# Optimization experiments

Hardware: AMD Instinct MI355X
Metric: run time of the kernel (lower is better)

The kernel has to match this reference:

```python
import jax, jax.numpy as jnp
import numpy as np

B, S, F, DV, H, DH, L = 32, 600, 9, 1024, 16, 64, 2


def setup_inputs() -> dict:
    key = jax.random.key(0)
    ks = jax.random.split(key, 24)
    w = lambda k, shape, s=0.05: jax.random.normal(k, shape, dtype=jnp.float32) * s
    return {
        "x": w(ks[0], (B, S, F), 1.0),
        "enc_in_W": w(ks[1], (F, DV)), "enc_in_b": w(ks[2], (DV,)),
        "Wq": w(ks[3], (L, H, DV, DH)), "bq": w(ks[4], (L, H, DH)),
        "Wk": w(ks[5], (L, H, DV, DH)), "bk": w(ks[6], (L, H, DH)),
        "Wv": w(ks[7], (L, H, DV, DH)), "bv": w(ks[8], (L, H, DH)),
        "Wo": w(ks[9], (L, DV, DV)), "bo": w(ks[10], (L, DV)),
        "W1": w(ks[11], (L, DV, DV)), "b1": w(ks[12], (L, DV)),
        "W2": w(ks[13], (L, DV, DV)), "b2": w(ks[14], (L, DV)),
        "ln1_w": jnp.ones((L, DV)), "ln1_b": jnp.zeros((L, DV)),
        "ln2_w": jnp.ones((L, DV)), "ln2_b": jnp.zeros((L, DV)),
        "out_W": w(ks[15], (DV, F)), "out_b": w(ks[16], (F,)),
    }


def _layernorm(v, g, b):
    mu = v.mean(-1, keepdims=True)
    var = v.var(-1, keepdims=True)  # biased, matches torch LayerNorm
    return (v - mu) / jnp.sqrt(var + 1e-5) * g + b


def reference(x, enc_in_W, enc_in_b, Wq, bq, Wk, bk, Wv, bv, Wo, bo,
              W1, b1, W2, b2, ln1_w, ln1_b, ln2_w, ln2_b, out_W, out_b):
    # enc_input_fc; pe skipped (code checks pe_mode == 'stardard', never true)
    h = x @ enc_in_W + enc_in_b  # [B,S,DV]
    scale = 1.0 / jnp.sqrt(jnp.float32(DH))
    for l in range(L):
        q = jnp.einsum('bsd,hdk->bhsk', h, Wq[l]) + bq[l][None, :, None, :]
        k = jnp.einsum('bsd,hdk->bhsk', h, Wk[l]) + bk[l][None, :, None, :]
        v = jnp.einsum('bsd,hdk->bhsk', h, Wv[l]) + bv[l][None, :, None, :]
        attn = jax.nn.softmax(jnp.einsum('bhsk,bhtk->bhst', q, k) * scale, axis=-1)
        ctx = jnp.einsum('bhst,bhtk->bhsk', attn, v)  # [B,H,S,DH]
        # torch: stack(heads, dim=-1) -> [B,S,DH,H], then flatten(start_dim=2)
        a = ctx.transpose(0, 2, 3, 1).reshape(B, S, DH * H)
        attn_out = a @ Wo[l] + bo[l]
        x1 = _layernorm(h + attn_out, ln1_w[l], ln1_b[l])
        ff = jax.nn.elu(x1 @ W2[l] + b2[l]) @ W1[l] + b1[l]  # fc1(elu(fc2(x1)))
        h = _layernorm(x1 + ff, ln2_w[l], ln2_b[l])
    out = h @ out_W + out_b  # [B,S,F]; in_seq_len == out_seq_len -> no out_seq_fc
    return out
```

## Files before the change

kernel.cpp:

```cpp
#include <hip/hip_runtime.h>

typedef unsigned short u16;
typedef unsigned int u32;
typedef __attribute__((ext_vector_type(8))) short shortx8;
typedef __attribute__((ext_vector_type(4))) float floatx4;
typedef __attribute__((ext_vector_type(4))) u32 uintx4;
typedef __attribute__((ext_vector_type(2))) u32 uintx2;

#define AS1 __attribute__((address_space(1)))
#define AS3 __attribute__((address_space(3)))

__device__ __forceinline__ float bf2f(u16 u) {
  return __builtin_bit_cast(float, ((u32)u) << 16);
}
__device__ __forceinline__ u16 f2bf(float f) {
  u32 i = __builtin_bit_cast(u32, f);
  u32 r = (i + 0x7fffu + ((i >> 16) & 1u)) >> 16;
  return (u16)r;
}
__device__ __forceinline__ u16 f2bf_rtz(float f) {
  return (u16)(__builtin_bit_cast(u32, f) >> 16);
}

__launch_bounds__(256)
__global__ void pack_all(const float* __restrict__ Wq, const float* __restrict__ Wk,
                         const float* __restrict__ Wv, const float* __restrict__ Wo,
                         const float* __restrict__ W1, const float* __restrict__ W2,
                         const float* __restrict__ bq, const float* __restrict__ bk,
                         const float* __restrict__ bv,
                         u16* __restrict__ Bqkv, u16* __restrict__ Bwo,
                         u16* __restrict__ Bw1, u16* __restrict__ Bw2,
                         float* __restrict__ bias) {
  __shared__ u16 T[64 * 72];
  const int blk = blockIdx.x;
  const int t = threadIdx.x;

  if (blk < 1536) {
    const int which = blk >> 9, r = blk & 511;
    const int kt = r & 15, y = r >> 4;
    const float* W = (which == 0) ? Wq : (which == 1) ? Wk : Wv;
    u16* dst = Bqkv + (size_t)which * 1048576;
    const int l = y >> 4, h = y & 15;
    const int rr = t >> 2, cq = (t & 3) * 16;
    const float* src = W + ((size_t)y * 1024 + kt * 64 + rr) * 64 + cq;
#pragma unroll
    for (int e4 = 0; e4 < 4; ++e4) {
      float4 f = *(const float4*)(src + e4 * 4);
      T[(cq + e4 * 4 + 0) * 72 + rr] = f2bf(f.x);
      T[(cq + e4 * 4 + 1) * 72 + rr] = f2bf(f.y);
      T[(cq + e4 * 4 + 2) * 72 + rr] = f2bf(f.z);
      T[(cq + e4 * 4 + 3) * 72 + rr] = f2bf(f.w);
    }
    __syncthreads();
    const int dd = t >> 2, kq = (t & 3) * 16;
    u16* drow = dst + (size_t)l * 3145728 + ((size_t)h * 64 + dd) * 1024 + kt * 64 + kq;
    *(uintx4*)(drow) = *(const uintx4*)&T[dd * 72 + kq];
    *(uintx4*)(drow + 8) = *(const uintx4*)&T[dd * 72 + kq + 8];
  } else if (blk < 2048) {
    const int r = blk - 1536;
    const int l = r >> 8, rx = r & 255;
    const int rt = rx >> 4, nt = rx & 15;
    const int rr = t >> 2, cq = (t & 3) * 16;
    const float* src = Wo + (size_t)l * 1048576 + (size_t)(rt * 64 + rr) * 1024 + nt * 64 + cq;
#pragma unroll
    for (int e4 = 0; e4 < 4; ++e4) {
      float4 f = *(const float4*)(src + e4 * 4);
      T[(cq + e4 * 4 + 0) * 72 + rr] = f2bf(f.x);
      T[(cq + e4 * 4 + 1) * 72 + rr] = f2bf(f.y);
      T[(cq + e4 * 4 + 2) * 72 + rr] = f2bf(f.z);
      T[(cq + e4 * 4 + 3) * 72 + rr] = f2bf(f.w);
    }
    __syncthreads();
    const int hh = t & 15;
#pragma unroll
    for (int pass = 0; pass < 4; ++pass) {
      const int nl = pass * 16 + (t >> 4);
      uintx2 pk;
      u16 v0 = T[nl * 72 + 0 * 16 + hh], v1 = T[nl * 72 + 1 * 16 + hh];
      u16 v2 = T[nl * 72 + 2 * 16 + hh], v3 = T[nl * 72 + 3 * 16 + hh];
      pk[0] = (u32)v0 | ((u32)v1 << 16);
      pk[1] = (u32)v2 | ((u32)v3 << 16);
      *(uintx2*)&Bwo[(size_t)l * 1048576 + (size_t)(nt * 64 + nl) * 1024 + hh * 64 + rt * 4] = pk;
    }
  } else if (blk < 3072) {
    const int job = (blk - 2048) >> 9;
    const int r = (blk - 2048) & 511;
    const float* W = job == 0 ? W1 : W2;
    u16* dst = job == 0 ? Bw1 : Bw2;
    const int l = r >> 8, rx = r & 255;
    const int ct = rx & 15, rt = rx >> 4;
    const int rr = t >> 2, cq = (t & 3) * 16;
    const float* src = W + (size_t)l * 1048576 + (size_t)(rt * 64 + rr) * 1024 + ct * 64 + cq;
#pragma unroll
    for (int e4 = 0; e4 < 4; ++e4) {
      float4 f = *(const float4*)(src + e4 * 4);
      T[(cq + e4 * 4 + 0) * 72 + rr] = f2bf(f.x);
      T[(cq + e4 * 4 + 1) * 72 + rr] = f2bf(f.y);
      T[(cq + e4 * 4 + 2) * 72 + rr] = f2bf(f.z);
      T[(cq + e4 * 4 + 3) * 72 + rr] = f2bf(f.w);
    }
    __syncthreads();
    const int cc = t >> 2, rq = (t & 3) * 16;
    u16* drow = dst + (size_t)l * 1048576 + (size_t)(ct * 64 + cc) * 1024 + rt * 64 + rq;
    *(uintx4*)(drow) = *(const uintx4*)&T[cc * 72 + rq];
    *(uintx4*)(drow + 8) = *(const uintx4*)&T[cc * 72 + rq + 8];
  } else {
    const int i = (blk - 3072) * 256 + t;
    const int l = i / 3072, n = i % 3072;
    const int which = n >> 10, nn = n & 1023;
    const float* s = (which == 0) ? bq : (which == 1) ? bk : bv;
    bias[i] = s[l * 1024 + nn];
  }
}

__launch_bounds__(256)
__global__ void enc_kernel(const float* __restrict__ x, const float* __restrict__ W,
                           const float* __restrict__ bias, u16* __restrict__ h) {
  const size_t i = (size_t)blockIdx.x * 256 + threadIdx.x;
  const int m = (int)(i >> 7), nq = (int)((i & 127) << 3);
  const float* xr = x + (size_t)m * 9;
  float xv[9];
#pragma unroll
  for (int f = 0; f < 9; ++f) xv[f] = xr[f];
  u16 ov[8];
#pragma unroll
  for (int e = 0; e < 8; ++e) {
    float acc = bias[nq + e];
#pragma unroll
    for (int f = 0; f < 9; ++f) acc += xv[f] * W[f * 1024 + nq + e];
    ov[e] = f2bf(acc);
  }
  *(uintx4*)&h[(size_t)m * 1024 + nq] = *(const uintx4*)ov;
}

template <int EPI>
__launch_bounds__(512)
__global__ void gemm_bt_wide(const u16* __restrict__ A, int lda,
                             const u16* __restrict__ Bt,
                             const float* __restrict__ bias,
                             const u16* __restrict__ R, int ldr,
                             u16* __restrict__ C, int ldc) {
  constexpr int K = 1024;
  __shared__ u16 As[128 * 64];
  __shared__ u16 Bs[256 * 64];
  const int tid = threadIdx.x;
  const int lane = tid & 63;
  const int w = tid >> 6;
  const int wr = w >> 2, wc = w & 3;
  const int m0 = blockIdx.y * 128, n0 = blockIdx.x * 256;

  floatx4 acc[4][4];
#pragma unroll
  for (int i = 0; i < 4; ++i)
#pragma unroll
    for (int j = 0; j < 4; ++j) acc[i][j] = (floatx4){0.f, 0.f, 0.f, 0.f};

  const u16* Ab = A + (size_t)m0 * lda;
  const u16* Bb = Bt + (size_t)n0 * K;

  for (int k0 = 0; k0 < K; k0 += 64) {
#pragma unroll
    for (int p = 0; p < 2; ++p) {
      const int o = p * 8192 + tid * 16;
      const int row = o >> 7;
      const int ke = (o & 127) >> 1;
      __builtin_amdgcn_global_load_lds((const AS1 void*)(Ab + (size_t)row * lda + (k0 + ke)),
                                       (AS3 void*)((char*)As + o), 16, 0, 0);
    }
#pragma unroll
    for (int p = 0; p < 4; ++p) {
      const int o = p * 8192 + tid * 16;
      const int row = o >> 7;
      const int ke = (o & 127) >> 1;
      __builtin_amdgcn_global_load_lds((const AS1 void*)(Bb + (size_t)row * K + (k0 + ke)),
                                       (AS3 void*)((char*)Bs + o), 16, 0, 0);
    }
    __syncthreads();
#pragma unroll
    for (int ks = 0; ks < 2; ++ks) {
      shortx8 af[4], bfr[4];
#pragma unroll
      for (int i = 0; i < 4; ++i) {
        const int ar = wr * 64 + i * 16 + (lane & 15);
        af[i] = *(const shortx8*)&As[ar * 64 + ks * 32 + (lane >> 4) * 8];
        const int br = wc * 64 + i * 16 + (lane & 15);
        bfr[i] = *(const shortx8*)&Bs[br * 64 + ks * 32 + (lane >> 4) * 8];
      }
#pragma unroll
      for (int i = 0; i < 4; ++i)
#pragma unroll
        for (int j = 0; j < 4; ++j)
          acc[i][j] = __builtin_amdgcn_mfma_f32_16x16x32_bf16(af[i], bfr[j], acc[i][j], 0, 0, 0);
    }
    __syncthreads();
  }

  const int lr = (lane >> 4) * 4, lc = lane & 15;
#pragma unroll
  for (int i = 0; i < 4; ++i) {
#pragma unroll
    for (int j = 0; j < 4; ++j) {
      const int col = n0 + wc * 64 + j * 16 + lc;
      const float bv = bias[col];
      const bool qcol = (EPI == 3) && (col < 1024);
#pragma unroll
      for (int r = 0; r < 4; ++r) {
        const int row = m0 + wr * 64 + i * 16 + lr + r;
        float v = acc[i][j][r] + bv;
        if (EPI == 1) v += bf2f(R[(size_t)row * ldr + col]);
        if (EPI == 2) v = v > 0.f ? v : expm1f(v);
        if (EPI == 3 && qcol) v *= 0.125f;
        C[(size_t)row * ldc + col] = f2bf(v);
      }
    }
  }
}

__launch_bounds__(256)
__global__ void attn_mfma(const u16* __restrict__ qkv, u16* __restrict__ aout) {
  const int qt = blockIdx.x, bh = blockIdx.y;
  const int b = bh >> 4, h = bh & 15;
  const int tid = threadIdx.x, lane = tid & 63, w = tid >> 6;
  const int g = lane >> 4, lq = lane & 15;

  __shared__ u16 K_ld[128 * 72];
  __shared__ u16 Vt[64 * 136];
  __shared__ u16 P_ld[4][16 * 136];

  const size_t bbase = (size_t)b * 600 * 3072;
  const int q0 = qt * 128 + w * 32;
  const int tloc = tid >> 1, dhalf = (tid & 1) * 32;
  const int dq = w * 16;

  shortx8 aq[2][2];
#pragma unroll
  for (int sub = 0; sub < 2; ++sub) {
    const int s = q0 + sub * 16 + lq;
    if (s < 600) {
      const u16* qp = qkv + bbase + (size_t)s * 3072 + h * 64 + g * 8;
      aq[sub][0] = *(const shortx8*)qp;
      aq[sub][1] = *(const shortx8*)(qp + 32);
    } else {
      aq[sub][0] = (shortx8){0, 0, 0, 0, 0, 0, 0, 0};
      aq[sub][1] = (shortx8){0, 0, 0, 0, 0, 0, 0, 0};
    }
  }

  floatx4 Oa[2][4];
  float m[2][4], l[2][4];
#pragma unroll
  for (int sub = 0; sub < 2; ++sub) {
#pragma unroll
    for (int db = 0; db < 4; ++db) Oa[sub][db] = (floatx4){0.f, 0.f, 0.f, 0.f};
#pragma unroll
    for (int r = 0; r < 4; ++r) { m[sub][r] = -1e30f; l[sub][r] = 0.f; }
  }

  uintx4 kreg[4];
  shortx8 vra, vrb, vrc, vrd;

  auto LOADC = [&](int ch) {
    const int t0 = ch * 128;
    if (ch < 4) {
      const u16* kp = qkv + bbase + (size_t)(t0 + tloc) * 3072 + 1024 + h * 64 + dhalf;
#pragma unroll
      for (int c = 0; c < 4; ++c) kreg[c] = *(const uintx4*)(kp + c * 8);
      const u16* vp0 = qkv + bbase + (size_t)(t0 + lane * 2) * 3072 + 2048 + h * 64 + dq;
      vra = *(const shortx8*)vp0;
      vrb = *(const shortx8*)(vp0 + 8);
      vrc = *(const shortx8*)(vp0 + 3072);
      vrd = *(const shortx8*)(vp0 + 3072 + 8);
    } else {
      const int tg = t0 + tloc;
      if (tg < 600) {
        const u16* kp = qkv + bbase + (size_t)tg * 3072 + 1024 + h * 64 + dhalf;
#pragma unroll
        for (int c = 0; c < 4; ++c) kreg[c] = *(const uintx4*)(kp + c * 8);
      } else {
#pragma unroll
        for (int c = 0; c < 4; ++c) kreg[c] = (uintx4){0, 0, 0, 0};
      }
      const int tp = t0 + lane * 2;
      if (tp < 600) {
        const u16* vp = qkv + bbase + (size_t)tp * 3072 + 2048 + h * 64 + dq;
        vra = *(const shortx8*)vp;
        vrb = *(const shortx8*)(vp + 8);
      } else {
        vra = (shortx8){0, 0, 0, 0, 0, 0, 0, 0};
        vrb = vra;
      }
      if (tp + 1 < 600) {
        const u16* vp = qkv + bbase + (size_t)(tp + 1) * 3072 + 2048 + h * 64 + dq;
        vrc = *(const shortx8*)vp;
        vrd = *(const shortx8*)(vp + 8);
      } else {
        vrc = (shortx8){0, 0, 0, 0, 0, 0, 0, 0};
        vrd = vrc;
      }
    }
  };
  auto WRITEC = [&]() {
#pragma unroll
    for (int c = 0; c < 4; ++c)
      *(uintx4*)&K_ld[tloc * 72 + dhalf + c * 8] = kreg[c];
#pragma unroll
    for (int e = 0; e < 8; ++e) {
      *(u32*)&Vt[(dq + e) * 136 + lane * 2] =
          (u32)(u16)vra[e] | ((u32)(u16)vrc[e] << 16);
      *(u32*)&Vt[(dq + 8 + e) * 136 + lane * 2] =
          (u32)(u16)vrb[e] | ((u32)(u16)vrd[e] << 16);
    }
  };

  LOADC(0);
  for (int ch = 0; ch < 5; ++ch) {
    const int t0 = ch * 128;
    __syncthreads();
    WRITEC();
    if (ch < 4) LOADC(ch + 1);
    __syncthreads();

#pragma unroll
    for (int sub = 0; sub < 2; ++sub) {
      floatx4 S[8];
      __builtin_amdgcn_s_setprio(1);
#pragma unroll
      for (int jb = 0; jb < 8; ++jb) {
        S[jb] = (floatx4){0.f, 0.f, 0.f, 0.f};
#pragma unroll
        for (int ks = 0; ks < 2; ++ks) {
          shortx8 bk = *(const shortx8*)&K_ld[(jb * 16 + lq) * 72 + ks * 32 + g * 8];
          S[jb] = __builtin_amdgcn_mfma_f32_16x16x32_bf16(aq[sub][ks], bk, S[jb], 0, 0, 0);
        }
      }
      __builtin_amdgcn_s_setprio(0);
      if (ch == 4) {
#pragma unroll
        for (int jb = 0; jb < 8; ++jb) {
          const bool ok = (t0 + jb * 16 + lq) < 600;
#pragma unroll
          for (int r = 0; r < 4; ++r) S[jb][r] = ok ? S[jb][r] : -1e30f;
        }
      }

      float vmax[4];
      bool need = false;
#pragma unroll
      for (int r = 0; r < 4; ++r) {
        const float v01 = fmaxf(S[0][r], S[1][r]);
        const float v23 = fmaxf(S[2][r], S[3][r]);
        const float v45 = fmaxf(S[4][r], S[5][r]);
        const float v67 = fmaxf(S[6][r], S[7][r]);
        float v = fmaxf(fmaxf(v01, v23), fmaxf(v45, v67));
        v = fmaxf(v, __shfl_xor(v, 1));
        v = fmaxf(v, __shfl_xor(v, 2));
        v = fmaxf(v, __shfl_xor(v, 4));
        v = fmaxf(v, __shfl_xor(v, 8));
        vmax[r] = v;
        need |= (v > m[sub][r] + 8.0f);
      }
      if (__any(need ? 1 : 0)) {
#pragma unroll
        for (int r = 0; r < 4; ++r) {
          const float mn = fmaxf(m[sub][r], vmax[r]);
          const float sc = __expf(m[sub][r] - mn);
          m[sub][r] = mn;
          l[sub][r] *= sc;
#pragma unroll
          for (int db = 0; db < 4; ++db) Oa[sub][db][r] *= sc;
        }
      }

      float sums[4] = {0.f, 0.f, 0.f, 0.f};
#pragma unroll
      for (int jb = 0; jb < 8; ++jb)
#pragma unroll
        for (int r = 0; r < 4; ++r) {
          const float p = __expf(S[jb][r] - m[sub][r]);
          sums[r] += p;
          P_ld[w][(g * 4 + r) * 136 + jb * 16 + lq] = f2bf_rtz(p);
        }
#pragma unroll
      for (int r = 0; r < 4; ++r) {
        float v = sums[r];
        v += __shfl_xor(v, 1);
        v += __shfl_xor(v, 2);
        v += __shfl_xor(v, 4);
        v += __shfl_xor(v, 8);
        l[sub][r] += v;
      }

      __builtin_amdgcn_s_setprio(1);
#pragma unroll
      for (int ks = 0; ks < 4; ++ks) {
        shortx8 ap = *(const shortx8*)&P_ld[w][lq * 136 + ks * 32 + g * 8];
#pragma unroll
        for (int db = 0; db < 4; ++db) {
          shortx8 bv = *(const shortx8*)&Vt[(db * 16 + lq) * 136 + ks * 32 + g * 8];
          Oa[sub][db] = __builtin_amdgcn_mfma_f32_16x16x32_bf16(ap, bv, Oa[sub][db], 0, 0, 0);
        }
      }
      __builtin_amdgcn_s_setprio(0);
    }
  }

#pragma unroll
  for (int sub = 0; sub < 2; ++sub) {
#pragma unroll
    for (int r = 0; r < 4; ++r) {
      const int sg = q0 + sub * 16 + g * 4 + r;
      if (sg < 600) {
        const float inv = 1.f / l[sub][r];
        u16* orow = aout + ((size_t)(b * 600 + sg)) * 1024 + h * 64;
#pragma unroll
        for (int db = 0; db < 4; ++db)
          orow[db * 16 + lq] = f2bf(Oa[sub][db][r] * inv);
      }
    }
  }
}

__launch_bounds__(256)
__global__ void ln_kernel(const u16* __restrict__ y, int ldy,
                          const float* __restrict__ g, const float* __restrict__ be,
                          u16* __restrict__ o, int ldo) {
  const int row = blockIdx.x, tid = threadIdx.x;
  const int lane = tid & 63, wv = tid >> 6;
  const u16* yr = y + (size_t)row * ldy;
  const int c = tid * 4;
  const uintx2 yv = *(const uintx2*)&yr[c];
  float v0 = bf2f((u16)(yv[0] & 0xffffu)), v1 = bf2f((u16)(yv[0] >> 16));
  float v2 = bf2f((u16)(yv[1] & 0xffffu)), v3 = bf2f((u16)(yv[1] >> 16));
  float s = v0 + v1 + v2 + v3;
  float q = v0 * v0 + v1 * v1 + v2 * v2 + v3 * v3;
#pragma unroll
  for (int m = 32; m; m >>= 1) {
    s += __shfl_xor(s, m);
    q += __shfl_xor(q, m);
  }
  __shared__ float red[2][4];
  if (lane == 0) {
    red[0][wv] = s;
    red[1][wv] = q;
  }
  __syncthreads();
  s = red[0][0] + red[0][1] + red[0][2] + red[0][3];
  q = red[1][0] + red[1][1] + red[1][2] + red[1][3];
  const float mu = s * (1.f / 1024.f);
  const float var = q * (1.f / 1024.f) - mu * mu;
  const float rstd = rsqrtf(var + 1e-5f);
  const float4 gv = *(const float4*)&g[c];
  const float4 bev = *(const float4*)&be[c];
  const float o0 = (v0 - mu) * rstd * gv.x + bev.x;
  const float o1 = (v1 - mu) * rstd * gv.y + bev.y;
  const float o2 = (v2 - mu) * rstd * gv.z + bev.z;
  const float o3 = (v3 - mu) * rstd * gv.w + bev.w;
  uintx2 ov;
  ov[0] = (u32)f2bf(o0) | ((u32)f2bf(o1) << 16);
  ov[1] = (u32)f2bf(o2) | ((u32)f2bf(o3) << 16);
  *(uintx2*)&o[(size_t)row * ldo + c] = ov;
}

__launch_bounds__(256)
__global__ void out_kernel(const u16* __restrict__ h, const float* __restrict__ W,
                           const float* __restrict__ bias, float* __restrict__ out) {
  const int m = blockIdx.x * 4 + (threadIdx.x >> 6);
  const int lane = threadIdx.x & 63;
  float acc[9];
#pragma unroll
  for (int f = 0; f < 9; ++f) acc[f] = 0.f;
  const u16* hr = h + (size_t)m * 1024;
#pragma unroll 4
  for (int j = 0; j < 16; ++j) {
    const int k = lane + j * 64;
    const float hv = bf2f(hr[k]);
    const float* wr = W + (size_t)k * 9;
#pragma unroll
    for (int f = 0; f < 9; ++f) acc[f] += hv * wr[f];
  }
#pragma unroll
  for (int f = 0; f < 9; ++f)
#pragma unroll
    for (int mm = 32; mm; mm >>= 1) acc[f] += __shfl_xor(acc[f], mm);
  if (lane < 9) out[(size_t)m * 9 + lane] = acc[lane] + bias[lane];
}

extern "C" void kernel_launch(void* const* d_in, const int* in_sizes, int n_in,
                              void* d_out, int out_size, void* d_ws, size_t ws_size,
                              hipStream_t stream) {
  (void)in_sizes; (void)n_in; (void)out_size; (void)ws_size;
  const float* x     = (const float*)d_in[0];
  const float* encW  = (const float*)d_in[1];
  const float* encB  = (const float*)d_in[2];
  const float* Wq    = (const float*)d_in[3];
  const float* bq    = (const float*)d_in[4];
  const float* Wk    = (const float*)d_in[5];
  const float* bk    = (const float*)d_in[6];
  const float* Wv    = (const float*)d_in[7];
  const float* bv    = (const float*)d_in[8];
  const float* Wo    = (const float*)d_in[9];
  const float* bo    = (const float*)d_in[10];
  const float* W1    = (const float*)d_in[11];
  const float* b1    = (const float*)d_in[12];
  const float* W2    = (const float*)d_in[13];
  const float* b2    = (const float*)d_in[14];
  const float* ln1w  = (const float*)d_in[15];
  const float* ln1b  = (const float*)d_in[16];
  const float* ln2w  = (const float*)d_in[17];
  const float* ln2b  = (const float*)d_in[18];
  const float* outW  = (const float*)d_in[19];
  const float* outB  = (const float*)d_in[20];
  float* out = (float*)d_out;

  char* ws = (char*)d_ws;
  size_t off = 0;
  auto alloc = [&](size_t bytes) -> void* {
    void* p = ws + off;
    off += (bytes + 255) & ~(size_t)255;
    return p;
  };
  u16* h    = (u16*)alloc(19660800ull * 2);
  u16* qkv  = (u16*)alloc(58982400ull * 2);
  u16* abuf = (u16*)alloc(19660800ull * 2);
  u16* Bqkv = (u16*)alloc(6291456ull * 2);
  u16* Bwo  = (u16*)alloc(2097152ull * 2);
  u16* Bw1  = (u16*)alloc(2097152ull * 2);
  u16* Bw2  = (u16*)alloc(2097152ull * 2);
  float* bqkv = (float*)alloc(6144ull * 4);
  u16* ybuf = qkv;
  u16* x1   = qkv + 1024;
  u16* mid  = qkv + 2048;
  u16* y2   = abuf;

  pack_all<<<3096, 256, 0, stream>>>(Wq, Wk, Wv, Wo, W1, W2, bq, bk, bv,
                                     Bqkv, Bwo, Bw1, Bw2, bqkv);
  enc_kernel<<<9600, 256, 0, stream>>>(x, encW, encB, h);

  for (int l = 0; l < 2; ++l) {
    gemm_bt_wide<3><<<dim3(12, 150), 512, 0, stream>>>(
        h, 1024, Bqkv + (size_t)l * 3145728, bqkv + l * 3072, nullptr, 0, qkv, 3072);
    attn_mfma<<<dim3(5, 512), 256, 0, stream>>>(qkv, abuf);
    gemm_bt_wide<1><<<dim3(4, 150), 512, 0, stream>>>(
        abuf, 1024, Bwo + (size_t)l * 1048576, bo + l * 1024, h, 1024, ybuf, 3072);
    ln_kernel<<<19200, 256, 0, stream>>>(ybuf, 3072, ln1w + l * 1024, ln1b + l * 1024, x1, 3072);
    gemm_bt_wide<2><<<dim3(4, 150), 512, 0, stream>>>(
        x1, 3072, Bw2 + (size_t)l * 1048576, b2 + l * 1024, nullptr, 0, mid, 3072);
    gemm_bt_wide<1><<<dim3(4, 150), 512, 0, stream>>>(
        mid, 3072, Bw1 + (size_t)l * 1048576, b1 + l * 1024, x1, 3072, y2, 1024);
    ln_kernel<<<19200, 256, 0, stream>>>(y2, 1024, ln2w + l * 1024, ln2b + l * 1024, h, 1024);
  }
  out_kernel<<<4800, 256, 0, stream>>>(h, outW, outB, out);
}
```

Baseline: 1.229 ms.

## Double attention query tile to 256 rows with 512-thread blocks sharing K/V chunks

The attention kernel now runs 8 waves per block covering 256 query rows instead of 4 waves covering 128, so each K/V chunk staged in LDS serves twice as many queries. The cooperative K/V load is split across 512 threads, each loading half as much. The grid drops from 5 to 3 query tiles per (batch, head), which cuts redundant global K/V reads. In exchange the last tile is mostly padding (768 rows for 600 queries), fewer blocks are launched, and LDS use per block grows.

```diff
diff --git a/kernel.cpp b/kernel.cpp
--- a/kernel.cpp
+++ b/kernel.cpp
@@ -216,7 +216,7 @@
   }
 }
 
-__launch_bounds__(256)
+__launch_bounds__(512)
 __global__ void attn_mfma(const u16* __restrict__ qkv, u16* __restrict__ aout) {
   const int qt = blockIdx.x, bh = blockIdx.y;
   const int b = bh >> 4, h = bh & 15;
@@ -225,12 +225,12 @@
 
   __shared__ u16 K_ld[128 * 72];
   __shared__ u16 Vt[64 * 136];
-  __shared__ u16 P_ld[4][16 * 136];
+  __shared__ u16 P_ld[8][16 * 136];
 
   const size_t bbase = (size_t)b * 600 * 3072;
-  const int q0 = qt * 128 + w * 32;
-  const int tloc = tid >> 1, dhalf = (tid & 1) * 32;
-  const int dq = w * 16;
+  const int q0 = qt * 256 + w * 32;
+  const int krow = tid >> 2, kseg = (tid & 3) * 16;
+  const int dv = w * 8;
 
   shortx8 aq[2][2];
 #pragma unroll
@@ -256,59 +256,50 @@
     for (int r = 0; r < 4; ++r) { m[sub][r] = -1e30f; l[sub][r] = 0.f; }
   }
 
-  uintx4 kreg[4];
-  shortx8 vra, vrb, vrc, vrd;
+  uintx4 kreg[2];
+  shortx8 vra, vrc;
 
   auto LOADC = [&](int ch) {
     const int t0 = ch * 128;
     if (ch < 4) {
-      const u16* kp = qkv + bbase + (size_t)(t0 + tloc) * 3072 + 1024 + h * 64 + dhalf;
-#pragma unroll
-      for (int c = 0; c < 4; ++c) kreg[c] = *(const uintx4*)(kp + c * 8);
-      const u16* vp0 = qkv + bbase + (size_t)(t0 + lane * 2) * 3072 + 2048 + h * 64 + dq;
-      vra = *(const shortx8*)vp0;
-      vrb = *(const shortx8*)(vp0 + 8);
-      vrc = *(const shortx8*)(vp0 + 3072);
-      vrd = *(const shortx8*)(vp0 + 3072 + 8);
+      const u16* kp = qkv + bbase + (size_t)(t0 + krow) * 3072 + 1024 + h * 64 + kseg;
+      kreg[0] = *(const uintx4*)kp;
+      kreg[1] = *(const uintx4*)(kp + 8);
+      const u16* vp = qkv + bbase + (size_t)(t0 + lane * 2) * 3072 + 2048 + h * 64 + dv;
+      vra = *(const shortx8*)vp;
+      vrc = *(const shortx8*)(vp + 3072);
     } else {
-      const int tg = t0 + tloc;
+      const int tg = t0 + krow;
       if (tg < 600) {
-        const u16* kp = qkv + bbase + (size_t)tg * 3072 + 1024 + h * 64 + dhalf;
-#pragma unroll
-        for (int c = 0; c < 4; ++c) kreg[c] = *(const uintx4*)(kp + c * 8);
+        const u16* kp = qkv + bbase + (size_t)tg * 3072 + 1024 + h * 64 + kseg;
+        kreg[0] = *(const uintx4*)kp;
+        kreg[1] = *(const uintx4*)(kp + 8);
       } else {
-#pragma unroll
-        for (int c = 0; c < 4; ++c) kreg[c] = (uintx4){0, 0, 0, 0};
+        kreg[0] = (uintx4){0, 0, 0, 0};
+        kreg[1] = kreg[0];
       }
       const int tp = t0 + lane * 2;
       if (tp < 600) {
-        const u16* vp = qkv + bbase + (size_t)tp * 3072 + 2048 + h * 64 + dq;
+        const u16* vp = qkv + bbase + (size_t)tp * 3072 + 2048 + h * 64 + dv;
         vra = *(const shortx8*)vp;
-        vrb = *(const shortx8*)(vp + 8);
       } else {
         vra = (shortx8){0, 0, 0, 0, 0, 0, 0, 0};
-        vrb = vra;
       }
       if (tp + 1 < 600) {
-        const u16* vp = qkv + bbase + (size_t)(tp + 1) * 3072 + 2048 + h * 64 + dq;
+        const u16* vp = qkv + bbase + (size_t)(tp + 1) * 3072 + 2048 + h * 64 + dv;
         vrc = *(const shortx8*)vp;
-        vrd = *(const shortx8*)(vp + 8);
       } else {
         vrc = (shortx8){0, 0, 0, 0, 0, 0, 0, 0};
-        vrd = vrc;
       }
     }
   };
   auto WRITEC = [&]() {
-#pragma unroll
-    for (int c = 0; c < 4; ++c)
-      *(uintx4*)&K_ld[tloc * 72 + dhalf + c * 8] = kreg[c];
+    *(uintx4*)&K_ld[krow * 72 + kseg] = kreg[0];
+    *(uintx4*)&K_ld[krow * 72 + kseg + 8] = kreg[1];
 #pragma unroll
     for (int e = 0; e < 8; ++e) {
-      *(u32*)&Vt[(dq + e) * 136 + lane * 2] =
+      *(u32*)&Vt[(dv + e) * 136 + lane * 2] =
           (u32)(u16)vra[e] | ((u32)(u16)vrc[e] << 16);
-      *(u32*)&Vt[(dq + 8 + e) * 136 + lane * 2] =
-          (u32)(u16)vrb[e] | ((u32)(u16)vrd[e] << 16);
     }
   };
 
@@ -539,7 +530,7 @@
   for (int l = 0; l < 2; ++l) {
     gemm_bt_wide<3><<<dim3(12, 150), 512, 0, stream>>>(
         h, 1024, Bqkv + (size_t)l * 3145728, bqkv + l * 3072, nullptr, 0, qkv, 3072);
-    attn_mfma<<<dim3(5, 512), 256, 0, stream>>>(qkv, abuf);
+    attn_mfma<<<dim3(3, 512), 512, 0, stream>>>(qkv, abuf);
     gemm_bt_wide<1><<<dim3(4, 150), 512, 0, stream>>>(
         abuf, 1024, Bwo + (size_t)l * 1048576, bo + l * 1024, h, 1024, ybuf, 3072);
     ln_kernel<<<19200, 256, 0, stream>>>(ybuf, 3072, ln1w + l * 1024, ln1b + l * 1024, x1, 3072);
```

New measurement: 1.280 ms. +4.2%, slower.
